# Kernel tuning notes

Hardware: AMD Instinct MI355X
Metric: run time of the kernel (lower is better)

## Reference

```python
import jax, jax.numpy as jnp
import numpy as np

B, N, D, H, F = 2, 2048, 1024, 16, 4096
E = D // H
EPS = 1e-5

def layer_norm(x, g, b):
    mu = jnp.mean(x, axis=-1, keepdims=True)
    var = jnp.var(x, axis=-1, keepdims=True)
    return (x - mu) * jax.lax.rsqrt(var + EPS) * g + b

def setup_inputs() -> dict:
    key = jax.random.key(0)
    ks = jax.random.split(key, 16)
    s = lambda k, sh, fan: jax.random.normal(k, sh, jnp.float32) * (1.0 / np.sqrt(fan))
    return {
        'x': jax.random.normal(ks[0], (B, N, D), jnp.float32),
        'wq': s(ks[1], (D, D), D), 'bq': jnp.zeros((D,), jnp.float32),
        'wk': s(ks[2], (D, D), D), 'bk': jnp.zeros((D,), jnp.float32),
        'wv': s(ks[3], (D, D), D), 'bv': jnp.zeros((D,), jnp.float32),
        'w1': s(ks[4], (F, D), D), 'b1': jnp.zeros((F,), jnp.float32),
        'ln_mlp_g': jnp.ones((F,), jnp.float32), 'ln_mlp_b': jnp.zeros((F,), jnp.float32),
        'w2': s(ks[5], (D, F), F), 'b2': jnp.zeros((D,), jnp.float32),
        'ln1_g': jnp.ones((D,), jnp.float32), 'ln1_b': jnp.zeros((D,), jnp.float32),
        'ln2_g': jnp.ones((D,), jnp.float32), 'ln2_b': jnp.zeros((D,), jnp.float32),
    }

def reference(x, wq, bq, wk, bk, wv, bv, w1, b1, ln_mlp_g, ln_mlp_b, w2, b2, ln1_g, ln1_b, ln2_g, ln2_b):
    h = layer_norm(x, ln1_g, ln1_b)                       # [B,N,D]
    q = (h @ wq.T + bq).reshape(B, N, H, E).transpose(0, 2, 1, 3)  # [B,H,N,E]
    k = (h @ wk.T + bk).reshape(B, N, H, E).transpose(0, 2, 1, 3)
    v = (h @ wv.T + bv).reshape(B, N, H, E).transpose(0, 2, 1, 3)
    # faithful to source: score = q@k^T / sqrt(1/emb_dim) == q@k^T * sqrt(emb_dim)
    score = jnp.einsum('bhne,bhme->bhnm', q, k) * np.sqrt(D).astype(np.float32)
    causal = jnp.tril(jnp.ones((N, N), bool))
    score = jnp.where(causal[None, None], score, -jnp.inf)
    weight = jax.nn.softmax(score, axis=-1)
    attn = jnp.einsum('bhnm,bhme->bhne', weight, v)       # [B,H,N,E]
    attn = attn.transpose(0, 2, 1, 3).reshape(B, N, D)
    x = x + attn
    h2 = layer_norm(x, ln2_g, ln2_b)
    m = h2 @ w1.T + b1                                    # [B,N,F]
    m = jax.nn.relu(layer_norm(m, ln_mlp_g, ln_mlp_b))
    # faithful: no second residual in the source forward
    return m @ w2.T + b2
```

## Files before the change

### kernel.cpp

```cpp
#include <hip/hip_runtime.h>
#include <cstdint>

typedef __bf16 bf16_t;
typedef bf16_t bf16x8 __attribute__((ext_vector_type(8)));
typedef bf16_t bf16x4 __attribute__((ext_vector_type(4)));
typedef float  floatx4 __attribute__((ext_vector_type(4)));

#define GLD_LDS(g, l) __builtin_amdgcn_global_load_lds( \
    (const __attribute__((address_space(1))) unsigned int*)(g), \
    (__attribute__((address_space(3))) unsigned int*)(l), 16, 0, 0)

#define MFMA_BF16_16x16x32 __builtin_amdgcn_mfma_f32_16x16x32_bf16

__global__ __launch_bounds__(256) void prep(
    const float* __restrict__ wq, const float* __restrict__ wk,
    const float* __restrict__ wv, const float* __restrict__ w1,
    const float* __restrict__ w2, const float* __restrict__ bq,
    const float* __restrict__ bk,
    bf16_t* __restrict__ wqk_hi, bf16_t* __restrict__ wqk_lo,
    bf16_t* __restrict__ wvb, bf16_t* __restrict__ w1b, bf16_t* __restrict__ w2b,
    float* __restrict__ bqk) {
  const int blk = blockIdx.x, tid = threadIdx.x;
  if (blk < 2048) {
    const int qk = blk >> 10;
    const int i  = (blk & 1023) * 256 + tid;
    const float* src = qk ? wk : wq;
    float4 v = ((const float4*)src)[i];
    float f[4] = {v.x, v.y, v.z, v.w};
    bf16x4 h, l;
    #pragma unroll
    for (int j = 0; j < 4; ++j) { h[j] = (bf16_t)f[j]; l[j] = (bf16_t)(f[j] - (float)h[j]); }
    ((bf16x4*)(wqk_hi + qk * 1024 * 1024))[i] = h;
    ((bf16x4*)(wqk_lo + qk * 1024 * 1024))[i] = l;
  } else if (blk < 3072) {
    const int i = (blk - 2048) * 256 + tid;
    float4 v = ((const float4*)wv)[i];
    bf16x4 o; o[0]=(bf16_t)v.x; o[1]=(bf16_t)v.y; o[2]=(bf16_t)v.z; o[3]=(bf16_t)v.w;
    ((bf16x4*)wvb)[i] = o;
  } else if (blk < 7168) {
    const int i = (blk - 3072) * 256 + tid;
    float4 v = ((const float4*)w1)[i];
    bf16x4 o; o[0]=(bf16_t)v.x; o[1]=(bf16_t)v.y; o[2]=(bf16_t)v.z; o[3]=(bf16_t)v.w;
    ((bf16x4*)w1b)[i] = o;
  } else if (blk < 11264) {
    const int i = (blk - 7168) * 256 + tid;
    float4 v = ((const float4*)w2)[i];
    bf16x4 o; o[0]=(bf16_t)v.x; o[1]=(bf16_t)v.y; o[2]=(bf16_t)v.z; o[3]=(bf16_t)v.w;
    ((bf16x4*)w2b)[i] = o;
  } else {
    const int i = (blk - 11264) * 256 + tid;
    if (i < 1024) { bqk[i] = bq[i]; bqk[1024 + i] = bk[i]; }
  }
}


__device__ __forceinline__ void block_sum2(float& s, float& ss, float* red) {
  #pragma unroll
  for (int off = 32; off > 0; off >>= 1) {
    s  += __shfl_down(s, off);
    ss += __shfl_down(ss, off);
  }
  const int wave = threadIdx.x >> 6;
  if ((threadIdx.x & 63) == 0) { red[wave * 2] = s; red[wave * 2 + 1] = ss; }
  __syncthreads();
  s  = red[0] + red[2] + red[4] + red[6];
  ss = red[1] + red[3] + red[5] + red[7];
}

__global__ __launch_bounds__(256) void ln_fwd_split(const float* __restrict__ x,
    const float* __restrict__ g, const float* __restrict__ b,
    bf16_t* __restrict__ out_hi, bf16_t* __restrict__ out_lo) {
  __shared__ float red[8];
  const size_t row = blockIdx.x;
  float4 v = ((const float4*)(x + row * 1024))[threadIdx.x];
  float s  = v.x + v.y + v.z + v.w;
  float ss = v.x*v.x + v.y*v.y + v.z*v.z + v.w*v.w;
  block_sum2(s, ss, red);
  const float mu  = s * (1.f / 1024.f);
  const float var = ss * (1.f / 1024.f) - mu * mu;
  const float rs  = rsqrtf(var + 1e-5f);
  float4 gg = ((const float4*)g)[threadIdx.x];
  float4 bb = ((const float4*)b)[threadIdx.x];
  float f[4];
  f[0] = (v.x - mu) * rs * gg.x + bb.x;
  f[1] = (v.y - mu) * rs * gg.y + bb.y;
  f[2] = (v.z - mu) * rs * gg.z + bb.z;
  f[3] = (v.w - mu) * rs * gg.w + bb.w;
  bf16x4 oh, ol;
  #pragma unroll
  for (int j = 0; j < 4; ++j) {
    oh[j] = (bf16_t)f[j];
    ol[j] = (bf16_t)(f[j] - (float)oh[j]);
  }
  ((bf16x4*)(out_hi + row * 1024))[threadIdx.x] = oh;
  ((bf16x4*)(out_lo + row * 1024))[threadIdx.x] = ol;
}

__global__ __launch_bounds__(256) void resid_ln_fwd(const float* __restrict__ x,
    const float* __restrict__ a, const float* __restrict__ g, const float* __restrict__ b,
    bf16_t* __restrict__ out) {
  __shared__ float red[8];
  const size_t row = blockIdx.x;
  float4 v = ((const float4*)(x + row * 1024))[threadIdx.x];
  float4 av = ((const float4*)(a + row * 1024))[threadIdx.x];
  v.x += av.x; v.y += av.y; v.z += av.z; v.w += av.w;
  float s  = v.x + v.y + v.z + v.w;
  float ss = v.x*v.x + v.y*v.y + v.z*v.z + v.w*v.w;
  block_sum2(s, ss, red);
  const float mu  = s * (1.f / 1024.f);
  const float var = ss * (1.f / 1024.f) - mu * mu;
  const float rs  = rsqrtf(var + 1e-5f);
  float4 gg = ((const float4*)g)[threadIdx.x];
  float4 bb = ((const float4*)b)[threadIdx.x];
  bf16x4 o;
  o[0] = (bf16_t)((v.x - mu) * rs * gg.x + bb.x);
  o[1] = (bf16_t)((v.y - mu) * rs * gg.y + bb.y);
  o[2] = (bf16_t)((v.z - mu) * rs * gg.z + bb.z);
  o[3] = (bf16_t)((v.w - mu) * rs * gg.w + bb.w);
  ((bf16x4*)(out + row * 1024))[threadIdx.x] = o;
}

__global__ __launch_bounds__(256) void ln_relu_inplace(bf16_t* __restrict__ m,
    const float* __restrict__ g, const float* __restrict__ b) {
  __shared__ float red[8];
  const size_t row = blockIdx.x;
  bf16_t* mr = m + row * 4096;
  const int base = threadIdx.x * 16;
  bf16x8 v0 = *(bf16x8*)(mr + base);
  bf16x8 v1 = *(bf16x8*)(mr + base + 8);
  float f[16];
  #pragma unroll
  for (int i = 0; i < 8; ++i) { f[i] = (float)v0[i]; f[8 + i] = (float)v1[i]; }
  float s = 0.f, ss = 0.f;
  #pragma unroll
  for (int i = 0; i < 16; ++i) { s += f[i]; ss += f[i] * f[i]; }
  block_sum2(s, ss, red);
  const float mu  = s * (1.f / 4096.f);
  const float var = ss * (1.f / 4096.f) - mu * mu;
  const float rs  = rsqrtf(var + 1e-5f);
  bf16x8 o0, o1;
  #pragma unroll
  for (int i = 0; i < 16; ++i) {
    float ov = (f[i] - mu) * rs * g[base + i] + b[base + i];
    ov = fmaxf(ov, 0.f);
    if (i < 8) o0[i] = (bf16_t)ov; else o1[i - 8] = (bf16_t)ov;
  }
  *(bf16x8*)(mr + base) = o0;
  *(bf16x8*)(mr + base + 8) = o1;
}

template <int OUT_MODE, int BM>
__global__ __launch_bounds__(256) void gemm_bt(
    const bf16_t* __restrict__ A, const bf16_t* __restrict__ Bw,
    const float* __restrict__ bias, void* __restrict__ Cp,
    int M, int N, int K) {
  constexpr int MI = BM / 32;
  __shared__ bf16_t As[BM * 32];
  __shared__ bf16_t Bs[128 * 32];
  const int tid  = threadIdx.x;
  const int wave = tid >> 6, lane = tid & 63;
  const int quad = lane >> 4, l15 = lane & 15;
  const int m0 = blockIdx.x * BM, n0 = blockIdx.y * 128;
  const int wm = (wave >> 1) * (BM / 2), wn = (wave & 1) * 64;
  const int srowA = wave * (BM / 4) + (lane >> 2);
  const int srowB = wave * 32 + (lane >> 2);
  const int scol = (lane & 3) * 8;

  floatx4 acc[MI][4] = {};

  const bf16_t* Ag = A  + (size_t)(m0 + srowA) * K + scol;
  const bf16_t* Bg = Bw + (size_t)(n0 + srowB) * K + scol;

  for (int k0 = 0; k0 < K; k0 += 32) {
    __syncthreads();
    #pragma unroll
    for (int i = 0; i < BM / 64; ++i)
      GLD_LDS(Ag + (size_t)(i * 16) * K + k0, As + wave * (BM / 4) * 32 + i * 512);
    #pragma unroll
    for (int i = 0; i < 2; ++i)
      GLD_LDS(Bg + (size_t)(i * 16) * K + k0, Bs + wave * 1024 + i * 512);
    __syncthreads();
    bf16x8 af[MI], bfr[4];
    #pragma unroll
    for (int i = 0; i < MI; ++i)
      af[i] = *(const bf16x8*)(As + (wm + i * 16 + l15) * 32 + quad * 8);
    #pragma unroll
    for (int j = 0; j < 4; ++j)
      bfr[j] = *(const bf16x8*)(Bs + (wn + j * 16 + l15) * 32 + quad * 8);
    #pragma unroll
    for (int i = 0; i < MI; ++i)
      #pragma unroll
      for (int j = 0; j < 4; ++j)
        acc[i][j] = MFMA_BF16_16x16x32(af[i], bfr[j], acc[i][j], 0, 0, 0);
  }
  #pragma unroll
  for (int j = 0; j < 4; ++j) {
    const int col = n0 + wn + j * 16 + l15;
    const float bv = bias[col];
    #pragma unroll
    for (int i = 0; i < MI; ++i) {
      #pragma unroll
      for (int r = 0; r < 4; ++r) {
        const int row = m0 + wm + i * 16 + quad * 4 + r;
        const float v = acc[i][j][r] + bv;
        if (OUT_MODE == 0) {
          ((float*)Cp)[(size_t)row * N + col] = v;
        } else if (OUT_MODE == 1) {
          ((bf16_t*)Cp)[(size_t)row * N + col] = (bf16_t)v;
        } else {
          const int b = row >> 11, n = row & 2047;
          const int h = col >> 6, e = col & 63;
          ((bf16_t*)Cp)[(((size_t)((b << 4) + h) * 2048 + n) << 6) + e] = (bf16_t)v;
        }
      }
    }
  }
}

__global__ __launch_bounds__(256) void gemm_qk_split(
    const bf16_t* __restrict__ Ah, const bf16_t* __restrict__ Al,
    const bf16_t* __restrict__ Bh, const bf16_t* __restrict__ Bl,
    const float* __restrict__ bias,
    bf16_t* __restrict__ qhi, bf16_t* __restrict__ qlo,
    bf16_t* __restrict__ khi, bf16_t* __restrict__ klo,
    int M, int N, int K) {
  __shared__ bf16_t Ash[64 * 32];
  __shared__ bf16_t Asl[64 * 32];
  __shared__ bf16_t Bsh[128 * 32];
  __shared__ bf16_t Bsl[128 * 32];
  const int tid  = threadIdx.x;
  const int wave = tid >> 6, lane = tid & 63;
  const int quad = lane >> 4, l15 = lane & 15;
  const int m0 = blockIdx.x * 64, n0 = blockIdx.y * 128;
  const int wm = (wave >> 1) * 32, wn = (wave & 1) * 64;
  const int srowA = wave * 16 + (lane >> 2);
  const int srowB = wave * 32 + (lane >> 2);
  const int scol = (lane & 3) * 8;

  floatx4 acc[2][4] = {};

  const size_t aoff = (size_t)(m0 + srowA) * K + scol;
  const size_t boff = (size_t)(n0 + srowB) * K + scol;

  for (int k0 = 0; k0 < K; k0 += 32) {
    __syncthreads();
    GLD_LDS(Ah + aoff + k0, Ash + wave * 512);
    GLD_LDS(Al + aoff + k0, Asl + wave * 512);
    #pragma unroll
    for (int i = 0; i < 2; ++i) {
      const size_t gb = boff + (size_t)(i * 16) * K + k0;
      GLD_LDS(Bh + gb, Bsh + wave * 1024 + i * 512);
      GLD_LDS(Bl + gb, Bsl + wave * 1024 + i * 512);
    }
    __syncthreads();
    bf16x8 ah[2], al[2], bh[4], bl[4];
    #pragma unroll
    for (int i = 0; i < 2; ++i) {
      const int ro = (wm + i * 16 + l15) * 32 + quad * 8;
      ah[i] = *(const bf16x8*)(Ash + ro);
      al[i] = *(const bf16x8*)(Asl + ro);
    }
    #pragma unroll
    for (int j = 0; j < 4; ++j) {
      const int ro = (wn + j * 16 + l15) * 32 + quad * 8;
      bh[j] = *(const bf16x8*)(Bsh + ro);
      bl[j] = *(const bf16x8*)(Bsl + ro);
    }
    #pragma unroll
    for (int i = 0; i < 2; ++i)
      #pragma unroll
      for (int j = 0; j < 4; ++j) {
        acc[i][j] = MFMA_BF16_16x16x32(ah[i], bh[j], acc[i][j], 0, 0, 0);
        acc[i][j] = MFMA_BF16_16x16x32(ah[i], bl[j], acc[i][j], 0, 0, 0);
        acc[i][j] = MFMA_BF16_16x16x32(al[i], bh[j], acc[i][j], 0, 0, 0);
      }
  }
  #pragma unroll
  for (int j = 0; j < 4; ++j) {
    const int col = n0 + wn + j * 16 + l15;
    const float bv = bias[col];
    const bool isq = col < 1024;
    bf16_t* hib = isq ? qhi : khi;
    bf16_t* lob = isq ? qlo : klo;
    const float scale = isq ? 32.0f : 1.0f;
    const int h = (col >> 6) & 15, e = col & 63;
    #pragma unroll
    for (int i = 0; i < 2; ++i) {
      #pragma unroll
      for (int r = 0; r < 4; ++r) {
        const int row = m0 + wm + i * 16 + quad * 4 + r;
        const int b = row >> 11, n = row & 2047;
        const float c = (acc[i][j][r] + bv) * scale;
        const bf16_t chi = (bf16_t)c;
        const bf16_t clo = (bf16_t)(c - (float)chi);
        const size_t dst = (((size_t)((b << 4) + h) * 2048 + n) << 6) + e;
        hib[dst] = chi;
        lob[dst] = clo;
      }
    }
  }
}

__global__ __launch_bounds__(256) void transpose_v(
    const bf16_t* __restrict__ vhm, bf16_t* __restrict__ vT) {
  __shared__ bf16_t T[64 * 72];
  const int bh = blockIdx.x, n0 = blockIdx.y * 64;
  const int r = threadIdx.x >> 2;
  const int c = (threadIdx.x & 3) * 16;
  const bf16_t* src = vhm + ((size_t)bh * 2048 + n0 + r) * 64 + c;
  bf16x8 a0 = *(const bf16x8*)src;
  bf16x8 a1 = *(const bf16x8*)(src + 8);
  #pragma unroll
  for (int j = 0; j < 8; ++j) {
    T[(c + j) * 72 + r]     = a0[j];
    T[(c + 8 + j) * 72 + r] = a1[j];
  }
  __syncthreads();
  bf16x8 o0 = *(const bf16x8*)(T + r * 72 + c);
  bf16x8 o1 = *(const bf16x8*)(T + r * 72 + c + 8);
  bf16_t* dst = vT + ((size_t)(bh * 64 + r)) * 2048 + n0 + c;
  *(bf16x8*)dst = o0;
  *(bf16x8*)(dst + 8) = o1;
}

__global__ __launch_bounds__(256, 4) void attn_causal(
    const bf16_t* __restrict__ qhi, const bf16_t* __restrict__ qlo,
    const bf16_t* __restrict__ khi, const bf16_t* __restrict__ klo,
    const bf16_t* __restrict__ vT, float* __restrict__ o) {
  __shared__ bf16_t KsH[64 * 72];
  __shared__ bf16_t KsL[64 * 72];
  __shared__ bf16_t Vt[64 * 72];
  __shared__ bf16_t Ps[4][16 * 70];

  const int tid  = threadIdx.x;
  const int wave = tid >> 6, lane = tid & 63;
  const int quad = lane >> 4, l15 = lane & 15;
  const int bh = blockIdx.x;
  const int q0 = (31 - (int)blockIdx.y) * 64;
  const size_t hb = (size_t)bh * 2048;

  const int wmin = q0 + wave * 16;
  const int qrow = wmin + l15;
  bf16x8 qh[2], ql[2];
  {
    const bf16_t* qbh = qhi + ((hb + wmin + l15) << 6) + quad * 8;
    const bf16_t* qbl = qlo + ((hb + wmin + l15) << 6) + quad * 8;
    qh[0] = *(const bf16x8*)qbh;
    qh[1] = *(const bf16x8*)(qbh + 32);
    ql[0] = *(const bf16x8*)qbl;
    ql[1] = *(const bf16x8*)(qbl + 32);
  }

  floatx4 accO[4] = {};
  float m_row = -1e30f;
  float l_row = 0.f;

  const int kr = wave * 16 + (lane >> 3);
  const int kc = (lane & 7) * 8;
  const bf16_t* kgh = khi + ((hb + kr) << 6) + kc;
  const bf16_t* kgl = klo + ((hb + kr) << 6) + kc;
  const bf16_t* vg  = vT + ((size_t)(bh * 64 + kr)) * 2048 + kc;

  bf16x8 pkh0 = *(const bf16x8*)(kgh);
  bf16x8 pkh1 = *(const bf16x8*)(kgh + (8 << 6));
  bf16x8 pkl0 = *(const bf16x8*)(kgl);
  bf16x8 pkl1 = *(const bf16x8*)(kgl + (8 << 6));
  bf16x8 pv0  = *(const bf16x8*)(vg);
  bf16x8 pv1  = *(const bf16x8*)(vg + 8 * 2048);

  const int ntiles = (q0 >> 6) + 1;
  for (int t = 0; t < ntiles; ++t) {
    const int k0 = t * 64;
    __syncthreads();
    *(bf16x8*)(KsH + kr * 72 + kc)       = pkh0;
    *(bf16x8*)(KsH + (kr + 8) * 72 + kc) = pkh1;
    *(bf16x8*)(KsL + kr * 72 + kc)       = pkl0;
    *(bf16x8*)(KsL + (kr + 8) * 72 + kc) = pkl1;
    *(bf16x8*)(Vt  + kr * 72 + kc)       = pv0;
    *(bf16x8*)(Vt  + (kr + 8) * 72 + kc) = pv1;
    if (t + 1 < ntiles) {
      const int koff = (t + 1) << 12;
      pkh0 = *(const bf16x8*)(kgh + koff);
      pkh1 = *(const bf16x8*)(kgh + koff + (8 << 6));
      pkl0 = *(const bf16x8*)(kgl + koff);
      pkl1 = *(const bf16x8*)(kgl + koff + (8 << 6));
      pv0  = *(const bf16x8*)(vg + (t + 1) * 64);
      pv1  = *(const bf16x8*)(vg + (t + 1) * 64 + 8 * 2048);
    }
    __syncthreads();

    const bool needmask = (k0 + 63 > wmin);

    floatx4 sv[4];
    #pragma unroll
    for (int j = 0; j < 4; ++j) {
      const bf16_t* kbh = KsH + (j * 16 + l15) * 72;
      const bf16_t* kbl = KsL + (j * 16 + l15) * 72;
      const bf16x8 kh0 = *(const bf16x8*)(kbh + quad * 8);
      const bf16x8 kh1 = *(const bf16x8*)(kbh + 32 + quad * 8);
      const bf16x8 kl0 = *(const bf16x8*)(kbl + quad * 8);
      const bf16x8 kl1 = *(const bf16x8*)(kbl + 32 + quad * 8);
      floatx4 acc = {};
      acc = MFMA_BF16_16x16x32(kh0, qh[0], acc, 0, 0, 0);
      acc = MFMA_BF16_16x16x32(kh1, qh[1], acc, 0, 0, 0);
      acc = MFMA_BF16_16x16x32(kl0, qh[0], acc, 0, 0, 0);
      acc = MFMA_BF16_16x16x32(kl1, qh[1], acc, 0, 0, 0);
      acc = MFMA_BF16_16x16x32(kh0, ql[0], acc, 0, 0, 0);
      acc = MFMA_BF16_16x16x32(kh1, ql[1], acc, 0, 0, 0);
      sv[j] = acc;
    }

    const int lim = qrow - k0 - quad * 4;
    float mr = -1e30f;
    #pragma unroll
    for (int j = 0; j < 4; ++j)
      #pragma unroll
      for (int r = 0; r < 4; ++r) {
        float x = sv[j][r];
        if (needmask && (j * 16 + r > lim)) x = -1e30f;
        sv[j][r] = x;
        mr = fmaxf(mr, x);
      }
    mr = fmaxf(mr, __shfl_xor(mr, 16));
    mr = fmaxf(mr, __shfl_xor(mr, 32));
    const float mold = m_row;
    const float mnew = fmaxf(mold, mr);
    m_row = mnew;
    float psum = 0.f;
    bf16x4 pb[4];
    #pragma unroll
    for (int j = 0; j < 4; ++j)
      #pragma unroll
      for (int r = 0; r < 4; ++r) {
        const float p = __expf(sv[j][r] - mnew);
        const bf16_t pv = (bf16_t)p;
        psum += (float)pv;
        pb[j][r] = pv;
      }
    {
      bf16_t* pw = &Ps[wave][l15 * 70];
      #pragma unroll
      for (int j = 0; j < 4; ++j)
        *(bf16x4*)(pw + j * 16 + quad * 4) = pb[j];
    }
    psum += __shfl_xor(psum, 16);
    psum += __shfl_xor(psum, 32);
    const float alpha = __expf(mold - mnew);
    l_row = l_row * alpha + psum;
    if (__any(mnew > mold)) {
      #pragma unroll
      for (int r = 0; r < 4; ++r) {
        const float ar = __shfl(alpha, quad * 4 + r);
        #pragma unroll
        for (int j = 0; j < 4; ++j) accO[j][r] *= ar;
      }
    }
    asm volatile("s_waitcnt lgkmcnt(0)" ::: "memory");

    bf16x8 pf[2];
    {
      const bf16_t* pr = &Ps[wave][l15 * 70];
      pf[0] = *(const bf16x8*)(pr + quad * 8);
      pf[1] = *(const bf16x8*)(pr + 32 + quad * 8);
    }
    #pragma unroll
    for (int j = 0; j < 4; ++j) {
      const bf16_t* vb = Vt + (j * 16 + l15) * 72;
      const bf16x8 vf0 = *(const bf16x8*)(vb + quad * 8);
      const bf16x8 vf1 = *(const bf16x8*)(vb + 32 + quad * 8);
      accO[j] = MFMA_BF16_16x16x32(pf[0], vf0, accO[j], 0, 0, 0);
      accO[j] = MFMA_BF16_16x16x32(pf[1], vf1, accO[j], 0, 0, 0);
    }
  }

  const int b = bh >> 4, h = bh & 15;
  #pragma unroll
  for (int r = 0; r < 4; ++r) {
    const float lr = __shfl(l_row, quad * 4 + r);
    const float linv = 1.f / lr;
    const int qr = wmin + quad * 4 + r;
    float* orow = o + ((size_t)(b * 2048) + qr) * 1024 + h * 64;
    #pragma unroll
    for (int j = 0; j < 4; ++j)
      orow[j * 16 + l15] = accO[j][r] * linv;
  }
}


extern "C" void kernel_launch(void* const* d_in, const int* in_sizes, int n_in,
                              void* d_out, int out_size, void* d_ws, size_t ws_size,
                              hipStream_t stream) {
  const float* x        = (const float*)d_in[0];
  const float* wq       = (const float*)d_in[1];
  const float* bq       = (const float*)d_in[2];
  const float* wk       = (const float*)d_in[3];
  const float* bk       = (const float*)d_in[4];
  const float* wv       = (const float*)d_in[5];
  const float* bv       = (const float*)d_in[6];
  const float* w1       = (const float*)d_in[7];
  const float* b1       = (const float*)d_in[8];
  const float* ln_mlp_g = (const float*)d_in[9];
  const float* ln_mlp_b = (const float*)d_in[10];
  const float* w2       = (const float*)d_in[11];
  const float* b2       = (const float*)d_in[12];
  const float* ln1_g    = (const float*)d_in[13];
  const float* ln1_b    = (const float*)d_in[14];
  const float* ln2_g    = (const float*)d_in[15];
  const float* ln2_b    = (const float*)d_in[16];

  char* ws = (char*)d_ws;
  bf16_t* h_hi   = (bf16_t*)(ws);
  bf16_t* h_lo   = (bf16_t*)(ws + (8u  << 20));
  bf16_t* vTb    = (bf16_t*)(ws);
  bf16_t* wqk_hi = (bf16_t*)(ws + (16u << 20));
  bf16_t* wqk_lo = (bf16_t*)(ws + (20u << 20));
  bf16_t* wvb    = (bf16_t*)(ws + (24u << 20));
  float*  bqk    = (float*) (ws + (26u << 20));
  bf16_t* w1b    = (bf16_t*)(ws + (28u << 20));
  bf16_t* w2b    = (bf16_t*)(ws + (36u << 20));
  bf16_t* qhi    = (bf16_t*)(ws + (44u << 20));
  bf16_t* qlo    = (bf16_t*)(ws + (52u << 20));
  bf16_t* khi    = (bf16_t*)(ws + (60u << 20));
  bf16_t* klo    = (bf16_t*)(ws + (68u << 20));
  bf16_t* mbuf   = (bf16_t*)(ws + (44u << 20));
  bf16_t* vhm    = (bf16_t*)(ws + (76u << 20));
  float*  attnb  = (float*) (ws + (84u << 20));
  bf16_t* h2     = (bf16_t*)(ws + (100u << 20));

  prep<<<11268, 256, 0, stream>>>(wq, wk, wv, w1, w2, bq, bk,
                                  wqk_hi, wqk_lo, wvb, w1b, w2b, bqk);

  ln_fwd_split<<<4096, 256, 0, stream>>>(x, ln1_g, ln1_b, h_hi, h_lo);
  gemm_qk_split<<<dim3(64, 16), 256, 0, stream>>>(h_hi, h_lo, wqk_hi, wqk_lo, bqk,
                                                  qhi, qlo, khi, klo, 4096, 2048, 1024);
  gemm_bt<2, 64><<<dim3(64, 8), 256, 0, stream>>>(h_hi, wvb, bv, vhm, 4096, 1024, 1024);
  transpose_v<<<dim3(32, 32), 256, 0, stream>>>(vhm, vTb);
  attn_causal<<<dim3(32, 32), 256, 0, stream>>>(qhi, qlo, khi, klo, vTb, attnb);
  resid_ln_fwd<<<4096, 256, 0, stream>>>(x, attnb, ln2_g, ln2_b, h2);
  gemm_bt<1, 128><<<dim3(32, 32), 256, 0, stream>>>(h2, w1b, b1, mbuf, 4096, 4096, 1024);
  ln_relu_inplace<<<4096, 256, 0, stream>>>(mbuf, ln_mlp_g, ln_mlp_b);
  gemm_bt<0, 64><<<dim3(64, 8), 256, 0, stream>>>(mbuf, w2b, b2, d_out, 4096, 1024, 4096);

  (void)in_sizes; (void)n_in; (void)out_size; (void)ws_size;
}
```

Baseline: 472.8 us.

## Load K/V MFMA fragments directly from global memory, dropping LDS staging

The attention kernel no longer stages K-hi, K-lo and V^T tiles through shared memory with two block barriers per tile. Each wave now reads its MFMA operand fragments straight from global memory (relying on L1/L2 for reuse across the four waves), and the occupancy hint rises from 4 to 5 blocks per CU. This removes barriers and LDS traffic, but each K/V tile is fetched four times per block through the cache, the register prefetch of the next tile is lost, and load latency is exposed directly ahead of the MFMAs.

```diff
diff --git a/kernel.cpp b/kernel.cpp
--- a/kernel.cpp
+++ b/kernel.cpp
@@ -323,13 +323,10 @@
   *(bf16x8*)(dst + 8) = o1;
 }
 
-__global__ __launch_bounds__(256, 4) void attn_causal(
+__global__ __launch_bounds__(256, 5) void attn_causal(
     const bf16_t* __restrict__ qhi, const bf16_t* __restrict__ qlo,
     const bf16_t* __restrict__ khi, const bf16_t* __restrict__ klo,
     const bf16_t* __restrict__ vT, float* __restrict__ o) {
-  __shared__ bf16_t KsH[64 * 72];
-  __shared__ bf16_t KsL[64 * 72];
-  __shared__ bf16_t Vt[64 * 72];
   __shared__ bf16_t Ps[4][16 * 70];
 
   const int tid  = threadIdx.x;
@@ -355,51 +352,24 @@
   float m_row = -1e30f;
   float l_row = 0.f;
 
-  const int kr = wave * 16 + (lane >> 3);
-  const int kc = (lane & 7) * 8;
-  const bf16_t* kgh = khi + ((hb + kr) << 6) + kc;
-  const bf16_t* kgl = klo + ((hb + kr) << 6) + kc;
-  const bf16_t* vg  = vT + ((size_t)(bh * 64 + kr)) * 2048 + kc;
-
-  bf16x8 pkh0 = *(const bf16x8*)(kgh);
-  bf16x8 pkh1 = *(const bf16x8*)(kgh + (8 << 6));
-  bf16x8 pkl0 = *(const bf16x8*)(kgl);
-  bf16x8 pkl1 = *(const bf16x8*)(kgl + (8 << 6));
-  bf16x8 pv0  = *(const bf16x8*)(vg);
-  bf16x8 pv1  = *(const bf16x8*)(vg + 8 * 2048);
+  const bf16_t* kghb = khi + ((hb + l15) << 6) + quad * 8;
+  const bf16_t* kglb = klo + ((hb + l15) << 6) + quad * 8;
+  const bf16_t* vgb  = vT + ((size_t)(bh * 64 + l15)) * 2048 + quad * 8;
 
   const int ntiles = (q0 >> 6) + 1;
   for (int t = 0; t < ntiles; ++t) {
     const int k0 = t * 64;
-    __syncthreads();
-    *(bf16x8*)(KsH + kr * 72 + kc)       = pkh0;
-    *(bf16x8*)(KsH + (kr + 8) * 72 + kc) = pkh1;
-    *(bf16x8*)(KsL + kr * 72 + kc)       = pkl0;
-    *(bf16x8*)(KsL + (kr + 8) * 72 + kc) = pkl1;
-    *(bf16x8*)(Vt  + kr * 72 + kc)       = pv0;
-    *(bf16x8*)(Vt  + (kr + 8) * 72 + kc) = pv1;
-    if (t + 1 < ntiles) {
-      const int koff = (t + 1) << 12;
-      pkh0 = *(const bf16x8*)(kgh + koff);
-      pkh1 = *(const bf16x8*)(kgh + koff + (8 << 6));
-      pkl0 = *(const bf16x8*)(kgl + koff);
-      pkl1 = *(const bf16x8*)(kgl + koff + (8 << 6));
-      pv0  = *(const bf16x8*)(vg + (t + 1) * 64);
-      pv1  = *(const bf16x8*)(vg + (t + 1) * 64 + 8 * 2048);
-    }
-    __syncthreads();
-
     const bool needmask = (k0 + 63 > wmin);
 
     floatx4 sv[4];
     #pragma unroll
     for (int j = 0; j < 4; ++j) {
-      const bf16_t* kbh = KsH + (j * 16 + l15) * 72;
-      const bf16_t* kbl = KsL + (j * 16 + l15) * 72;
-      const bf16x8 kh0 = *(const bf16x8*)(kbh + quad * 8);
-      const bf16x8 kh1 = *(const bf16x8*)(kbh + 32 + quad * 8);
-      const bf16x8 kl0 = *(const bf16x8*)(kbl + quad * 8);
-      const bf16x8 kl1 = *(const bf16x8*)(kbl + 32 + quad * 8);
+      const bf16_t* kbh = kghb + ((size_t)(k0 + j * 16) << 6);
+      const bf16_t* kbl = kglb + ((size_t)(k0 + j * 16) << 6);
+      const bf16x8 kh0 = *(const bf16x8*)kbh;
+      const bf16x8 kh1 = *(const bf16x8*)(kbh + 32);
+      const bf16x8 kl0 = *(const bf16x8*)kbl;
+      const bf16x8 kl1 = *(const bf16x8*)(kbl + 32);
       floatx4 acc = {};
       acc = MFMA_BF16_16x16x32(kh0, qh[0], acc, 0, 0, 0);
       acc = MFMA_BF16_16x16x32(kh1, qh[1], acc, 0, 0, 0);
@@ -465,9 +435,9 @@
     }
     #pragma unroll
     for (int j = 0; j < 4; ++j) {
-      const bf16_t* vb = Vt + (j * 16 + l15) * 72;
-      const bf16x8 vf0 = *(const bf16x8*)(vb + quad * 8);
-      const bf16x8 vf1 = *(const bf16x8*)(vb + 32 + quad * 8);
+      const bf16_t* vb = vgb + (size_t)(j * 16) * 2048 + k0;
+      const bf16x8 vf0 = *(const bf16x8*)vb;
+      const bf16x8 vf1 = *(const bf16x8*)(vb + 32);
       accO[j] = MFMA_BF16_16x16x32(pf[0], vf0, accO[j], 0, 0, 0);
       accO[j] = MFMA_BF16_16x16x32(pf[1], vf1, accO[j], 0, 0, 0);
     }
```

New measurement: 588.2 us. +24.4%, slower.
